# Optimization experiments

Measured on AMD Instinct MI355X. Metric: run time of the kernel, lower is better.

Reference implementation:

```python
import jax, jax.numpy as jnp
import numpy as np


def setup_inputs() -> dict:
    key = jax.random.key(0)
    x = jax.random.normal(key, (4096, 512), dtype=jnp.float32)
    return {"x": x}


def reference(x):
    # Pairwise Euclidean distances for all (i, j) with i > j, flattened in the
    # same order as the original nested loop: (1,0),(2,0),(2,1),(3,0),...
    n = x.shape[0]
    sq = jnp.sum(x * x, axis=1)                      # [N]
    gram = x @ x.T                                   # [N, N]
    d2 = sq[:, None] + sq[None, :] - 2.0 * gram      # [N, N] squared dists
    ii, jj = jnp.tril_indices(n, k=-1)               # row-major lower triangle
    return jnp.sqrt(jnp.maximum(d2[ii, jj], 0.0))    # [N*(N-1)/2]
```

## Files before the change

kernel.cpp:

```cpp
#include <hip/hip_runtime.h>
#include <hip/hip_bf16.h>
#include <stdint.h>

#define N 4096
#define D 512
#define TILE 128
#define KITERS 4
#define NB (N / TILE)

typedef float f32x4 __attribute__((ext_vector_type(4)));
typedef int   i32x8 __attribute__((ext_vector_type(8)));
typedef int   i32x4 __attribute__((ext_vector_type(4)));

__global__ __launch_bounds__(256) void prep_kernel(const float* __restrict__ x,
                                                   unsigned char* __restrict__ xq,
                                                   float* __restrict__ sq) {
    int row  = blockIdx.x * 4 + (threadIdx.x >> 6);
    int lane = threadIdx.x & 63;
    const float* xr = x + (size_t)row * D + lane * 8;
    float4 v0 = *reinterpret_cast<const float4*>(xr);
    float4 v1 = *reinterpret_cast<const float4*>(xr + 4);

    int w0 = __builtin_amdgcn_cvt_pk_fp8_f32(v0.x, v0.y, 0, false);
    w0     = __builtin_amdgcn_cvt_pk_fp8_f32(v0.z, v0.w, w0, true);
    int w1 = __builtin_amdgcn_cvt_pk_fp8_f32(v1.x, v1.y, 0, false);
    w1     = __builtin_amdgcn_cvt_pk_fp8_f32(v1.z, v1.w, w1, true);
    reinterpret_cast<int2*>(xq + (size_t)row * D)[lane] = make_int2(w0, w1);

    float s = v0.x * v0.x + v0.y * v0.y + v0.z * v0.z + v0.w * v0.w +
              v1.x * v1.x + v1.y * v1.y + v1.z * v1.z + v1.w * v1.w;
    #pragma unroll
    for (int off = 32; off > 0; off >>= 1) s += __shfl_down(s, off);
    if (lane == 0) sq[row] = s;
}

__global__ __launch_bounds__(256, 2) void pairdist_kernel(const unsigned char* __restrict__ xq,
                                                          const float* __restrict__ sq,
                                                          float* __restrict__ out) {
    int t  = blockIdx.x;
    int bi = (int)((sqrtf(8.0f * (float)t + 1.0f) - 1.0f) * 0.5f);
    while ((bi + 1) * (bi + 2) / 2 <= t) bi++;
    while (bi * (bi + 1) / 2 > t) bi--;
    int bj = t - bi * (bi + 1) / 2;

    int tid  = threadIdx.x;
    int w    = tid >> 6;
    int lane = tid & 63;
    int quad = lane >> 4;
    int lr   = lane & 15;
    int wm   = w >> 1;
    int wn   = w & 1;

    int ibase = bi * TILE + wm * 64;
    int jbase = bj * TILE + wn * 64;

    f32x4 acc[4][4];
    #pragma unroll
    for (int mt = 0; mt < 4; mt++)
        #pragma unroll
        for (int nt = 0; nt < 4; nt++)
            acc[mt][nt] = (f32x4)0.0f;

    const unsigned char* pa[4];
    const unsigned char* pb[4];
    #pragma unroll
    for (int mt = 0; mt < 4; mt++)
        pa[mt] = xq + (size_t)(ibase + mt * 16 + lr) * D + quad * 32;
    #pragma unroll
    for (int nt = 0; nt < 4; nt++)
        pb[nt] = xq + (size_t)(jbase + nt * 16 + lr) * D + quad * 32;

    #pragma unroll
    for (int it = 0; it < KITERS; ++it) {
        const int k0 = it * 128;
        i32x8 af[4], bfr[4];
        #pragma unroll
        for (int mt = 0; mt < 4; mt++) {
            i32x4 lo = *reinterpret_cast<const i32x4*>(pa[mt] + k0);
            i32x4 hi = *reinterpret_cast<const i32x4*>(pa[mt] + k0 + 16);
            af[mt][0] = lo[0]; af[mt][1] = lo[1]; af[mt][2] = lo[2]; af[mt][3] = lo[3];
            af[mt][4] = hi[0]; af[mt][5] = hi[1]; af[mt][6] = hi[2]; af[mt][7] = hi[3];
        }
        #pragma unroll
        for (int nt = 0; nt < 4; nt++) {
            i32x4 lo = *reinterpret_cast<const i32x4*>(pb[nt] + k0);
            i32x4 hi = *reinterpret_cast<const i32x4*>(pb[nt] + k0 + 16);
            bfr[nt][0] = lo[0]; bfr[nt][1] = lo[1]; bfr[nt][2] = lo[2]; bfr[nt][3] = lo[3];
            bfr[nt][4] = hi[0]; bfr[nt][5] = hi[1]; bfr[nt][6] = hi[2]; bfr[nt][7] = hi[3];
        }

        #pragma unroll
        for (int mt = 0; mt < 4; mt++)
            #pragma unroll
            for (int nt = 0; nt < 4; nt++)
                acc[mt][nt] = __builtin_amdgcn_mfma_scale_f32_16x16x128_f8f6f4(
                    af[mt], bfr[nt], acc[mt][nt],
                    0, 0,
                    0, 0x7F7F7F7F,
                    0, 0x7F7F7F7F);
    }

    float sqi[4][4], sqj[4];
    #pragma unroll
    for (int mt = 0; mt < 4; mt++)
        #pragma unroll
        for (int tt = 0; tt < 4; tt++)
            sqi[mt][tt] = sq[ibase + mt * 16 + quad * 4 + tt];
    #pragma unroll
    for (int nt = 0; nt < 4; nt++)
        sqj[nt] = sq[jbase + nt * 16 + lr];

    if (bi != bj) {
        #pragma unroll
        for (int mt = 0; mt < 4; mt++) {
            #pragma unroll
            for (int tt = 0; tt < 4; tt++) {
                int i = ibase + mt * 16 + quad * 4 + tt;
                unsigned rowoff = (unsigned)(i * (i - 1) / 2);
                #pragma unroll
                for (int nt = 0; nt < 4; nt++) {
                    int j = jbase + nt * 16 + lr;
                    float d2 = sqi[mt][tt] + sqj[nt] - 2.0f * acc[mt][nt][tt];
                    out[rowoff + (unsigned)j] = sqrtf(fmaxf(d2, 0.0f));
                }
            }
        }
    } else {
        #pragma unroll
        for (int mt = 0; mt < 4; mt++) {
            #pragma unroll
            for (int tt = 0; tt < 4; tt++) {
                int i = ibase + mt * 16 + quad * 4 + tt;
                unsigned rowoff = (unsigned)(i * (i - 1) / 2);
                #pragma unroll
                for (int nt = 0; nt < 4; nt++) {
                    int j = jbase + nt * 16 + lr;
                    if (j < i) {
                        float d2 = sqi[mt][tt] + sqj[nt] - 2.0f * acc[mt][nt][tt];
                        out[rowoff + (unsigned)j] = sqrtf(fmaxf(d2, 0.0f));
                    }
                }
            }
        }
    }
}

extern "C" void kernel_launch(void* const* d_in, const int* in_sizes, int n_in,
                              void* d_out, int out_size, void* d_ws, size_t ws_size,
                              hipStream_t stream) {
    const float* x = (const float*)d_in[0];
    float* out = (float*)d_out;

    unsigned char* xq = (unsigned char*)d_ws;
    float* sq = (float*)((char*)d_ws + (size_t)N * D);

    prep_kernel<<<N / 4, 256, 0, stream>>>(x, xq, sq);

    int nblocks = NB * (NB + 1) / 2;
    pairdist_kernel<<<nblocks, 256, 0, stream>>>(xq, sq, out);
}
```

Baseline: 99.14 us.

## Stage FP8 tiles through swizzled LDS with direct global-to-LDS loads

```diff
diff --git a/kernel.cpp b/kernel.cpp
--- a/kernel.cpp
+++ b/kernel.cpp
@@ -5,7 +5,7 @@
 #define N 4096
 #define D 512
 #define TILE 128
-#define KITERS 4
+#define BK 256
 #define NB (N / TILE)
 
 typedef float f32x4 __attribute__((ext_vector_type(4)));
@@ -37,6 +37,9 @@
 __global__ __launch_bounds__(256, 2) void pairdist_kernel(const unsigned char* __restrict__ xq,
                                                           const float* __restrict__ sq,
                                                           float* __restrict__ out) {
+    __shared__ __align__(16) unsigned char As[TILE * BK];
+    __shared__ __align__(16) unsigned char Bs[TILE * BK];
+
     int t  = blockIdx.x;
     int bi = (int)((sqrtf(8.0f * (float)t + 1.0f) - 1.0f) * 0.5f);
     while ((bi + 1) * (bi + 2) / 2 <= t) bi++;
@@ -54,52 +57,6 @@
     int ibase = bi * TILE + wm * 64;
     int jbase = bj * TILE + wn * 64;
 
-    f32x4 acc[4][4];
-    #pragma unroll
-    for (int mt = 0; mt < 4; mt++)
-        #pragma unroll
-        for (int nt = 0; nt < 4; nt++)
-            acc[mt][nt] = (f32x4)0.0f;
-
-    const unsigned char* pa[4];
-    const unsigned char* pb[4];
-    #pragma unroll
-    for (int mt = 0; mt < 4; mt++)
-        pa[mt] = xq + (size_t)(ibase + mt * 16 + lr) * D + quad * 32;
-    #pragma unroll
-    for (int nt = 0; nt < 4; nt++)
-        pb[nt] = xq + (size_t)(jbase + nt * 16 + lr) * D + quad * 32;
-
-    #pragma unroll
-    for (int it = 0; it < KITERS; ++it) {
-        const int k0 = it * 128;
-        i32x8 af[4], bfr[4];
-        #pragma unroll
-        for (int mt = 0; mt < 4; mt++) {
-            i32x4 lo = *reinterpret_cast<const i32x4*>(pa[mt] + k0);
-            i32x4 hi = *reinterpret_cast<const i32x4*>(pa[mt] + k0 + 16);
-            af[mt][0] = lo[0]; af[mt][1] = lo[1]; af[mt][2] = lo[2]; af[mt][3] = lo[3];
-            af[mt][4] = hi[0]; af[mt][5] = hi[1]; af[mt][6] = hi[2]; af[mt][7] = hi[3];
-        }
-        #pragma unroll
-        for (int nt = 0; nt < 4; nt++) {
-            i32x4 lo = *reinterpret_cast<const i32x4*>(pb[nt] + k0);
-            i32x4 hi = *reinterpret_cast<const i32x4*>(pb[nt] + k0 + 16);
-            bfr[nt][0] = lo[0]; bfr[nt][1] = lo[1]; bfr[nt][2] = lo[2]; bfr[nt][3] = lo[3];
-            bfr[nt][4] = hi[0]; bfr[nt][5] = hi[1]; bfr[nt][6] = hi[2]; bfr[nt][7] = hi[3];
-        }
-
-        #pragma unroll
-        for (int mt = 0; mt < 4; mt++)
-            #pragma unroll
-            for (int nt = 0; nt < 4; nt++)
-                acc[mt][nt] = __builtin_amdgcn_mfma_scale_f32_16x16x128_f8f6f4(
-                    af[mt], bfr[nt], acc[mt][nt],
-                    0, 0,
-                    0, 0x7F7F7F7F,
-                    0, 0x7F7F7F7F);
-    }
-
     float sqi[4][4], sqj[4];
     #pragma unroll
     for (int mt = 0; mt < 4; mt++)
@@ -109,6 +66,86 @@
     #pragma unroll
     for (int nt = 0; nt < 4; nt++)
         sqj[nt] = sq[jbase + nt * 16 + lr];
+
+    f32x4 acc[4][4];
+    #pragma unroll
+    for (int mt = 0; mt < 4; mt++)
+        #pragma unroll
+        for (int nt = 0; nt < 4; nt++)
+            acc[mt][nt] = (f32x4)0.0f;
+
+    int srow4 = lane >> 4;
+    int sch   = lane & 15;
+
+    const unsigned char* gaP[8];
+    const unsigned char* gbP[8];
+    #pragma unroll
+    for (int g = 0; g < 8; g++) {
+        int rw  = g * 4 + srow4;
+        int src = (sch ^ (rw & 15)) << 4;
+        gaP[g] = xq + (size_t)(bi * TILE + w * 32 + rw) * D + src;
+        gbP[g] = xq + (size_t)(bj * TILE + w * 32 + rw) * D + src;
+    }
+    unsigned char* la = As + w * 32 * BK;
+    unsigned char* lb = Bs + w * 32 * BK;
+
+#define STAGE(k0)                                                             \
+    do {                                                                      \
+        _Pragma("unroll")                                                     \
+        for (int g = 0; g < 8; g++) {                                         \
+            __builtin_amdgcn_global_load_lds(                                 \
+                (const __attribute__((address_space(1))) void*)(gaP[g] + (k0)), \
+                (__attribute__((address_space(3))) void*)(la + g * 4 * BK),   \
+                16, 0, 0);                                                    \
+            __builtin_amdgcn_global_load_lds(                                 \
+                (const __attribute__((address_space(1))) void*)(gbP[g] + (k0)), \
+                (__attribute__((address_space(3))) void*)(lb + g * 4 * BK),   \
+                16, 0, 0);                                                    \
+        }                                                                     \
+    } while (0)
+
+#define COMPUTE(s)                                                            \
+    do {                                                                      \
+        int c0 = ((((8 * (s) + 2 * quad) & 15) ^ lr) << 4);   \
+        int c1 = c0 ^ 16;                                                     \
+        i32x8 af[4], bfr[4];                                                  \
+        _Pragma("unroll")                                                     \
+        for (int mt = 0; mt < 4; mt++) {                                      \
+            const unsigned char* rb = As + (wm * 64 + mt * 16 + lr) * BK;     \
+            i32x4 lo = *reinterpret_cast<const i32x4*>(rb + c0);              \
+            i32x4 hi = *reinterpret_cast<const i32x4*>(rb + c1);              \
+            af[mt][0] = lo[0]; af[mt][1] = lo[1]; af[mt][2] = lo[2]; af[mt][3] = lo[3]; \
+            af[mt][4] = hi[0]; af[mt][5] = hi[1]; af[mt][6] = hi[2]; af[mt][7] = hi[3]; \
+        }                                                                     \
+        _Pragma("unroll")                                                     \
+        for (int nt = 0; nt < 4; nt++) {                                      \
+            const unsigned char* rb = Bs + (wn * 64 + nt * 16 + lr) * BK;     \
+            i32x4 lo = *reinterpret_cast<const i32x4*>(rb + c0);              \
+            i32x4 hi = *reinterpret_cast<const i32x4*>(rb + c1);              \
+            bfr[nt][0] = lo[0]; bfr[nt][1] = lo[1]; bfr[nt][2] = lo[2]; bfr[nt][3] = lo[3]; \
+            bfr[nt][4] = hi[0]; bfr[nt][5] = hi[1]; bfr[nt][6] = hi[2]; bfr[nt][7] = hi[3]; \
+        }                                                                     \
+        _Pragma("unroll")                                                     \
+        for (int mt = 0; mt < 4; mt++)                                        \
+            _Pragma("unroll")                                                 \
+            for (int nt = 0; nt < 4; nt++)                                    \
+                acc[mt][nt] = __builtin_amdgcn_mfma_scale_f32_16x16x128_f8f6f4( \
+                    af[mt], bfr[nt], acc[mt][nt],                             \
+                    0, 0, 0, 0x7F7F7F7F, 0, 0x7F7F7F7F);                      \
+    } while (0)
+
+    STAGE(0);
+    __syncthreads();
+    COMPUTE(0);
+    COMPUTE(1);
+    __syncthreads();
+    STAGE(256);
+    __syncthreads();
+    COMPUTE(2);
+    COMPUTE(3);
+
+#undef STAGE
+#undef COMPUTE
 
     if (bi != bj) {
         #pragma unroll
```

Result: faster. 84.25 us (-15.0%).
